# Optimization experiments

Hardware: AMD Instinct MI355X
Metric: run time of the kernel (lower is better)

## Reference

```python
import jax, jax.numpy as jnp
import numpy as np

N, E, B = 10000, 20000, 500
H, NODE_D, EDGE_D, L = 64, 11, 5, 3
BN_EPS = 1e-5
STEPS = 3  # Set2Set processing steps


def setup_inputs() -> dict:
    key = jax.random.key(0)
    ks = jax.random.split(key, 16)
    s = lambda k, shape, fan: (jax.random.normal(k, shape, jnp.float32) / np.sqrt(fan)).astype(jnp.float32)
    p = {}
    p["x"] = jax.random.normal(ks[0], (N, NODE_D), jnp.float32)
    p["edge_index"] = jax.random.randint(ks[1], (2, E), 0, N)
    p["edge_attr"] = jax.random.uniform(ks[2], (E, EDGE_D), dtype=jnp.float32)
    p["batch"] = jnp.sort(jax.random.randint(ks[3], (N,), 0, B))
    # node encoder
    p["W_enc"] = s(ks[4], (NODE_D, H), NODE_D); p["b_enc"] = jnp.zeros((H,), jnp.float32)
    # per-layer NNConv block params (stacked over L layers)
    p["eW1"] = s(ks[5], (L, EDGE_D, H), EDGE_D); p["eb1"] = jnp.zeros((L, H), jnp.float32)
    p["eW2"] = s(ks[6], (L, H, H * H), H);       p["eb2"] = jnp.zeros((L, H * H), jnp.float32)
    p["root"] = s(ks[7], (L, H, H), H);          p["cbias"] = jnp.zeros((L, H), jnp.float32)
    p["gamma"] = jnp.ones((L, H), jnp.float32);  p["beta"] = jnp.zeros((L, H), jnp.float32)
    # Set2Set LSTM (input 2H, hidden H)
    p["Wih"] = s(ks[8], (4 * H, 2 * H), 2 * H); p["Whh"] = s(ks[9], (4 * H, H), H)
    p["bih"] = jnp.zeros((4 * H,), jnp.float32); p["bhh"] = jnp.zeros((4 * H,), jnp.float32)
    p["hW1"] = s(ks[10], (2 * H, H), 2 * H);   p["hb1"] = jnp.zeros((H,), jnp.float32)
    p["hW2"] = s(ks[11], (H, H // 2), H);      p["hb2"] = jnp.zeros((H // 2,), jnp.float32)
    p["hW3"] = s(ks[12], (H // 2, 1), H // 2); p["hb3"] = jnp.zeros((1,), jnp.float32)
    return p


def _forward(x, edge_attr, W_enc, b_enc, eW1, eb1, eW2, eb2, root, cbias, gamma, beta,
             Wih, Whh, bih, bhh, hW1, hb1, hW2, hb2, hW3, hb3, edge_index, batch):
    src, dst = edge_index[0], edge_index[1]
    # in-degree for mean aggregation (0-degree nodes -> 0 output, clamp avoids /0)
    deg = jax.ops.segment_sum(jnp.ones((E,), jnp.float32), dst, num_segments=N)
    deg = jnp.maximum(deg, 1.0)[:, None]

    h = jax.nn.relu(x @ W_enc + b_enc)  # [N, H]

    for l in range(L):
        residual = h
        # edge MLP -> per-edge [H, H] weight matrix
        e1 = jax.nn.relu(edge_attr @ eW1[l] + eb1[l])          # [E, H]
        W = (e1 @ eW2[l] + eb2[l]).reshape(E, H, H)            # [E, H, H]
        msg = jnp.einsum('eh,eho->eo', h[src], W)              # per-edge matvec
        agg = jax.ops.segment_sum(msg, dst, num_segments=N) / deg
        h = agg + h @ root[l] + cbias[l]                       # NNConv (root + bias)
        # BatchNorm1d (training-mode batch stats, biased var), eval-mode dropout (no-op)
        mu = jnp.mean(h, axis=0)
        var = jnp.mean((h - mu) ** 2, axis=0)
        h = (h - mu) * jax.lax.rsqrt(var + BN_EPS) * gamma[l] + beta[l]
        h = jax.nn.relu(h) + residual

    # Set2Set readout
    q_star = jnp.zeros((B, 2 * H), jnp.float32)
    hl = jnp.zeros((B, H), jnp.float32)
    cl = jnp.zeros((B, H), jnp.float32)
    for _ in range(STEPS):
        gates = q_star @ Wih.T + bih + hl @ Whh.T + bhh
        i, f, g, o = jnp.split(gates, 4, axis=1)
        cl = jax.nn.sigmoid(f) * cl + jax.nn.sigmoid(i) * jnp.tanh(g)
        hl = jax.nn.sigmoid(o) * jnp.tanh(cl)
        q = hl                                                  # [B, H]
        e = jnp.sum(h * q[batch], axis=-1)                      # [N]
        m = jax.ops.segment_max(e, batch, num_segments=B)
        ex = jnp.exp(e - m[batch])
        sden = jax.ops.segment_sum(ex, batch, num_segments=B)
        a = ex / sden[batch]                                    # per-graph softmax
        r = jax.ops.segment_sum(a[:, None] * h, batch, num_segments=B)
        q_star = jnp.concatenate([q, r], axis=1)

    # head
    z = jax.nn.relu(q_star @ hW1 + hb1)
    z = jax.nn.relu(z @ hW2 + hb2)
    out = z @ hW3 + hb3
    return out.reshape(-1)  # [B]


def reference(x, edge_index, edge_attr, batch, W_enc, b_enc, eW1, eb1, eW2, eb2, root,
              cbias, gamma, beta, Wih, Whh, bih, bhh, hW1, hb1, hW2, hb2, hW3, hb3):
    return _forward(x, edge_attr, W_enc, b_enc, eW1, eb1, eW2, eb2, root, cbias, gamma,
                    beta, Wih, Whh, bih, bhh, hW1, hb1, hW2, hb2, hW3, hb3,
                    edge_index, batch)
```

## Files before the change

### kernel.cpp

```cpp
#include <hip/hip_runtime.h>
#include <math.h>

#define ND 11
#define ED 5
#define NL 3
#define NSTEPS 3
#define BN_EPS 1e-5f
#define NSLAB 32

typedef _Float16 half8 __attribute__((ext_vector_type(8)));
typedef float f32x4 __attribute__((ext_vector_type(4)));

__device__ __forceinline__ float sigm(float x) { return 1.0f / (1.0f + expf(-x)); }

__device__ __forceinline__ half8 to_h8(float4 a, float4 b) {
  half8 r;
  r[0] = (_Float16)a.x; r[1] = (_Float16)a.y; r[2] = (_Float16)a.z; r[3] = (_Float16)a.w;
  r[4] = (_Float16)b.x; r[5] = (_Float16)b.y; r[6] = (_Float16)b.z; r[7] = (_Float16)b.w;
  return r;
}

__device__ __forceinline__ half8 bn_h8(const float* __restrict__ hnrow,
                                       const float* __restrict__ hprow,
                                       const float* mu, const float* rs,
                                       const float* bt, int c0) {
  float4 p0 = *(const float4*)(hnrow);
  float4 p1 = *(const float4*)(hnrow + 4);
  float4 q0 = *(const float4*)(hprow);
  float4 q1 = *(const float4*)(hprow + 4);
  float pv[8] = {p0.x, p0.y, p0.z, p0.w, p1.x, p1.y, p1.z, p1.w};
  float qv[8] = {q0.x, q0.y, q0.z, q0.w, q1.x, q1.y, q1.z, q1.w};
  half8 r;
#pragma unroll
  for (int j = 0; j < 8; ++j) {
    float y = fmaxf((pv[j] - mu[c0 + j]) * rs[c0 + j] + bt[c0 + j], 0.f) + qv[j];
    r[j] = (_Float16)y;
  }
  return r;
}

__global__ __launch_bounds__(256) void k_setup(
    const float* __restrict__ x, const float* __restrict__ Wenc,
    const float* __restrict__ benc, float* __restrict__ h0, int N,
    const int* __restrict__ dst, float* __restrict__ deg, int E,
    const int* __restrict__ batch, int* __restrict__ ptr, int B,
    const float* __restrict__ Wih, const float* __restrict__ Whh,
    const float* __restrict__ bih, const float* __restrict__ bhh,
    float* __restrict__ WihT, float* __restrict__ WhhT, float* __restrict__ gbias,
    const float* __restrict__ w2, const float* __restrict__ b2,
    _Float16* __restrict__ w2P, float* __restrict__ zp, long NZ,
    int nbEnc, int nbDeg, int nbPtr, int nbPackW, int nbPack3) {
  int bid = blockIdx.x;
  const int tid = threadIdx.x;
  if (bid < nbEnc) {
    int idx = bid * 256 + tid;
    if (idx < N * 64) {
      int n = idx >> 6, j = idx & 63;
      float acc = benc[j];
#pragma unroll
      for (int i = 0; i < ND; ++i) acc = fmaf(x[n * ND + i], Wenc[i * 64 + j], acc);
      h0[idx] = fmaxf(acc, 0.0f);
    }
    return;
  }
  bid -= nbEnc;
  if (bid < nbDeg) {
    int e = bid * 256 + tid;
    if (e < E) atomicAdd(&deg[dst[e]], 1.0f);
    return;
  }
  bid -= nbDeg;
  if (bid < nbPtr) {
    int n = bid * 256 + tid;
    if (n < N) {
      int b = batch[n];
      int pb = (n == 0) ? -1 : batch[n - 1];
      for (int g = pb + 1; g <= b; ++g) ptr[g] = n;
      if (n == N - 1)
        for (int g = b + 1; g <= B; ++g) ptr[g] = N;
    }
    return;
  }
  bid -= nbPtr;
  if (bid < nbPackW) {
    int idx = bid * 256 + tid;
    if (idx < 128 * 256) {
      int i = idx >> 8, g = idx & 255;
      WihT[i * 256 + g] = Wih[g * 128 + i];
    } else if (idx < 192 * 256) {
      int j = idx - 128 * 256;
      int i = j >> 8, g = j & 255;
      WhhT[i * 256 + g] = Whh[g * 64 + i];
    } else if (idx < 192 * 256 + 256) {
      int g = idx - 192 * 256;
      gbias[g] = bih[g] + bhh[g];
    }
    return;
  }
  bid -= nbPackW;
  if (bid < nbPack3) {
    int lay = bid / 130;
    int idx = (bid % 130) * 256 + tid;
    int l = idx & 63;
    int f = (idx >> 6) & 7;
    int s = idx >> 9;
    int nf = f >> 1, kf = f & 1;
    const float* srow = (s < 64) ? (w2 + (size_t)lay * 64 * 4096 + (size_t)s * 4096)
                                 : (b2 + (size_t)lay * 4096);
    int o = nf * 16 + (l & 15);
    int hb = kf * 32 + (l >> 4) * 8;
    half8 v;
#pragma unroll
    for (int j = 0; j < 8; ++j) v[j] = (_Float16)srow[(hb + j) * 64 + o];
    *(half8*)(w2P + ((size_t)lay * 65 * 8 * 64 + idx) * 8) = v;
    return;
  }
  bid -= nbPack3;
  {
    long i4 = ((long)bid * 256 + tid) * 4;
    if (i4 + 3 < NZ) *(float4*)(zp + i4) = make_float4(0.f, 0.f, 0.f, 0.f);
    else for (; i4 < NZ; ++i4) zp[i4] = 0.f;
  }
}

__global__ void k_zdeg(float* __restrict__ deg, int N) {
  int i = blockIdx.x * blockDim.x + threadIdx.x;
  if (i < N) deg[i] = 0.f;
}

__global__ __launch_bounds__(256) void k_scan(const float* __restrict__ deg,
                                              int* __restrict__ dptr,
                                              int* __restrict__ cursor, int N) {
  __shared__ int wsum[4];
  __shared__ int s_carry;
  const int tid = threadIdx.x, lane = tid & 63, w = tid >> 6;
  if (tid == 0) s_carry = 0;
  __syncthreads();
  for (int base = 0; base < N; base += 1024) {
    int n0 = base + tid * 4;
    int v[4];
    int s = 0;
#pragma unroll
    for (int i = 0; i < 4; ++i) { v[i] = (n0 + i < N) ? (int)deg[n0 + i] : 0; s += v[i]; }
    int sc = s;
#pragma unroll
    for (int off = 1; off < 64; off <<= 1) {
      int t = __shfl_up(sc, off);
      if (lane >= off) sc += t;
    }
    if (lane == 63) wsum[w] = sc;
    __syncthreads();
    int wpre = 0;
    for (int ww = 0; ww < w; ++ww) wpre += wsum[ww];
    int excl = s_carry + wpre + sc - s;
#pragma unroll
    for (int i = 0; i < 4; ++i) {
      if (n0 + i < N) { dptr[n0 + i] = excl; cursor[n0 + i] = excl; }
      excl += v[i];
    }
    __syncthreads();
    if (tid == 255) s_carry += wsum[0] + wsum[1] + wsum[2] + wsum[3];
    __syncthreads();
  }
  if (threadIdx.x == 0) dptr[N] = s_carry;
}

__global__ void k_fill(const int* __restrict__ dst, const int* __restrict__ src,
                       int* __restrict__ cursor, int* __restrict__ perm,
                       int* __restrict__ srcP, int* __restrict__ dstP, int E) {
  int e = blockIdx.x * blockDim.x + threadIdx.x;
  if (e < E) {
    int d = dst[e];
    int slot = atomicAdd(&cursor[d], 1);
    perm[slot] = e;
    srcP[slot] = src[e];
    dstP[slot] = d;
  }
}

__global__ __launch_bounds__(512, 2) void k_msgagg(
    const float* __restrict__ ea, const int* __restrict__ perm,
    const float* __restrict__ eW1l, const float* __restrict__ eb1l,
    const float* __restrict__ hnp, const float* __restrict__ hp,
    const float* __restrict__ slabp, const float* __restrict__ gm,
    const float* __restrict__ bt, const int* __restrict__ srcP,
    const int* __restrict__ dstP, const int* __restrict__ dptr,
    const _Float16* __restrict__ w2P, float* __restrict__ agg, int E, int N) {
  __shared__ _Float16 e1t[65][64];
  __shared__ float tileH[2][64][66];
  __shared__ float eat[64][ED];
  __shared__ float w1s[ED * 64];
  __shared__ float b1s[64];
  __shared__ float stats[128];
  __shared__ float mu_s[64], rs_s[64], bt_s[64];

  const int tid = threadIdx.x;
  const int wid = tid >> 6, l = tid & 63;
  const int half = wid >> 2, quad = wid & 3;
  const int lo = l & 15, lg = l >> 4;
  const int e0 = blockIdx.x * 64;

  if (tid < ED * 64) w1s[tid] = eW1l[tid];
  else if (tid < ED * 64 + 64) b1s[tid - ED * 64] = eb1l[tid - ED * 64];
  else if (tid >= 384 && tid < 448 && slabp) {
    int j = tid - 384;
    float s0 = 0.f, s1 = 0.f;
#pragma unroll
    for (int sl = 0; sl < NSLAB; ++sl) {
      s0 += slabp[sl * 128 + j];
      s1 += slabp[sl * 128 + 64 + j];
    }
    stats[j] = s0;
    stats[64 + j] = s1;
  }
  if (tid >= 448) {
    int s = e0 + (tid - 448);
    if (s < E) {
      int e = perm[s];
#pragma unroll
      for (int i = 0; i < ED; ++i) eat[tid - 448][i] = ea[(size_t)e * ED + i];
    } else {
#pragma unroll
      for (int i = 0; i < ED; ++i) eat[tid - 448][i] = 0.f;
    }
  }
  __syncthreads();
  if (slabp && tid < 64) {
    float invN = 1.0f / (float)N;
    float mu = stats[tid] * invN;
    float var = stats[64 + tid] * invN - mu * mu;
    mu_s[tid] = mu;
    rs_s[tid] = rsqrtf(var + BN_EPS) * gm[tid];
    bt_s[tid] = bt[tid];
  }
  __syncthreads();

  for (int idx = tid; idx < 65 * 64; idx += 512) {
    int el = idx & 63, k = idx >> 6;
    float v = 1.0f;
    if (k < 64) {
      v = b1s[k];
#pragma unroll
      for (int i = 0; i < ED; ++i) v = fmaf(eat[el][i], w1s[i * 64 + k], v);
      v = fmaxf(v, 0.f);
    }
    e1t[k][el] = (_Float16)v;
  }

  half8 hsf[4][2];
#pragma unroll
  for (int m = 0; m < 4; ++m) {
    int s = e0 + m * 16 + lo;
    if (s < E) {
      const size_t row = (size_t)srcP[s] * 64;
      if (!slabp) {
        const float* hr = hp + row + lg * 8;
        hsf[m][0] = to_h8(*(const float4*)(hr), *(const float4*)(hr + 4));
        hsf[m][1] = to_h8(*(const float4*)(hr + 32), *(const float4*)(hr + 36));
      } else {
        hsf[m][0] = bn_h8(hnp + row + lg * 8, hp + row + lg * 8, mu_s, rs_s, bt_s, lg * 8);
        hsf[m][1] = bn_h8(hnp + row + 32 + lg * 8, hp + row + 32 + lg * 8,
                          mu_s, rs_s, bt_s, 32 + lg * 8);
      }
    } else {
      half8 z = {0, 0, 0, 0, 0, 0, 0, 0};
      hsf[m][0] = z;
      hsf[m][1] = z;
    }
  }
  __syncthreads();

  const int kb = half ? 32 : 0;
  f32x4 acc[4] = {};
  const half8* wp = (const half8*)w2P;
  half8 Br[4][2];
  _Float16 sr[4][4];
#pragma unroll
  for (int d = 0; d < 4; ++d) {
    const int k = kb + d;
    Br[d][0] = wp[((size_t)k * 8 + quad * 2 + 0) * 64 + l];
    Br[d][1] = wp[((size_t)k * 8 + quad * 2 + 1) * 64 + l];
#pragma unroll
    for (int m = 0; m < 4; ++m)
      sr[d][m] = (half && d == 0) ? (_Float16)0.f : e1t[k][m * 16 + lo];
  }
#pragma unroll 33
  for (int i = 0; i < 33; ++i) {
    const int d = i & 3;
#pragma unroll
    for (int m = 0; m < 4; ++m) {
      const _Float16 s16 = sr[d][m];
      half8 A0 = hsf[m][0] * s16;
      half8 A1 = hsf[m][1] * s16;
      acc[m] = __builtin_amdgcn_mfma_f32_16x16x32_f16(A0, Br[d][0], acc[m], 0, 0, 0);
      acc[m] = __builtin_amdgcn_mfma_f32_16x16x32_f16(A1, Br[d][1], acc[m], 0, 0, 0);
    }
    if (i + 4 < 33) {
      const int kn = kb + i + 4;
      Br[d][0] = wp[((size_t)kn * 8 + quad * 2 + 0) * 64 + l];
      Br[d][1] = wp[((size_t)kn * 8 + quad * 2 + 1) * 64 + l];
#pragma unroll
      for (int m = 0; m < 4; ++m) sr[d][m] = e1t[kn][m * 16 + lo];
    }
  }

#pragma unroll
  for (int m = 0; m < 4; ++m)
#pragma unroll
    for (int r = 0; r < 4; ++r)
      tileH[half][m * 16 + lg * 4 + r][quad * 16 + lo] = acc[m][r];
  __syncthreads();

  const int o = tid & 63, r8 = tid >> 6;
  const int lastSlot = (e0 + 63 < E) ? (e0 + 63) : (E - 1);
  const int nLo = dstP[e0], nHi = dstP[lastSlot];
  for (int nn = nLo + r8; nn <= nHi; nn += 8) {
    int d0 = dptr[nn], d1 = dptr[nn + 1];
    int j0 = (d0 > e0) ? d0 : e0;
    int j1 = (d1 < e0 + 64) ? d1 : (e0 + 64);
    float sum = 0.f;
    for (int j = j0; j < j1; ++j) sum += tileH[0][j - e0][o] + tileH[1][j - e0][o];
    float* dp = agg + (size_t)nn * 64 + o;
    if (d0 < e0 || d1 > e0 + 64) atomicAdd(dp, sum);
    else *dp = sum;
  }
}

__global__ __launch_bounds__(256) void k_update(
    const float* __restrict__ hnp, const float* __restrict__ hp,
    const float* __restrict__ slabp, const float* __restrict__ gm,
    const float* __restrict__ bt, float* __restrict__ hcur,
    float* __restrict__ agg, const float* __restrict__ deg,
    const float* __restrict__ root, const float* __restrict__ cb,
    float* __restrict__ hn_out, float* __restrict__ slab_out, int N) {
  __shared__ float hrow[16][64];
  __shared__ float red[2][256];
  __shared__ float stats[128];
  const int tid = threadIdx.x, o = tid & 63, r = tid >> 6;
  float muR = 0.f, rsR = 0.f, btR = 0.f;
  if (slabp) {
    if (tid < 128) {
      float s = 0.f;
#pragma unroll
      for (int sl = 0; sl < NSLAB; ++sl) s += slabp[sl * 128 + tid];
      stats[tid] = s;
    }
    __syncthreads();
    float invN = 1.0f / (float)N;
    float mu = stats[o] * invN;
    float var = stats[64 + o] * invN - mu * mu;
    muR = mu;
    rsR = rsqrtf(var + BN_EPS) * gm[o];
    btR = bt[o];
  }
  const int nb = blockIdx.x * 16;
#pragma unroll
  for (int ii = 0; ii < 4; ++ii) {
    int n = nb + ii * 4 + r;
    float hv = 0.f;
    if (n < N) {
      if (slabp) {
        float hnv = hnp[(size_t)n * 64 + o];
        float hpv = hp[(size_t)n * 64 + o];
        hv = fmaxf((hnv - muR) * rsR + btR, 0.f) + hpv;
        hcur[(size_t)n * 64 + o] = hv;
      } else {
        hv = hcur[(size_t)n * 64 + o];
      }
    }
    hrow[ii * 4 + r][o] = hv;
  }
  __syncthreads();
  float acc[4] = {0.f, 0.f, 0.f, 0.f};
  for (int c = 0; c < 64; ++c) {
    float rv = root[c * 64 + o];
#pragma unroll
    for (int ii = 0; ii < 4; ++ii) acc[ii] = fmaf(hrow[ii * 4 + r][c], rv, acc[ii]);
  }
  float s = 0.f, ss = 0.f;
  const float cbv = cb[o];
#pragma unroll
  for (int ii = 0; ii < 4; ++ii) {
    int n = nb + ii * 4 + r;
    if (n < N) {
      float a = agg[(size_t)n * 64 + o];
      agg[(size_t)n * 64 + o] = 0.f;
      float v = acc[ii] + cbv + a / fmaxf(deg[n], 1.0f);
      hn_out[(size_t)n * 64 + o] = v;
      s += v;
      ss += v * v;
    }
  }
  red[0][tid] = s;
  red[1][tid] = ss;
  __syncthreads();
  if (r == 0) {
    float t0 = red[0][o] + red[0][64 + o] + red[0][128 + o] + red[0][192 + o];
    float t1 = red[1][o] + red[1][64 + o] + red[1][128 + o] + red[1][192 + o];
    float* sl = slab_out + (size_t)(blockIdx.x & (NSLAB - 1)) * 128;
    atomicAdd(&sl[o], t0);
    atomicAdd(&sl[64 + o], t1);
  }
}

__global__ __launch_bounds__(256) void k_s2s_all(
    const float* __restrict__ hn2, const float* __restrict__ h2,
    const float* __restrict__ slab2, const float* __restrict__ gm,
    const float* __restrict__ bt, const int* __restrict__ ptr,
    const float* __restrict__ WihT, const float* __restrict__ WhhT,
    const float* __restrict__ gbias,
    const float* __restrict__ hW1, const float* __restrict__ hb1,
    const float* __restrict__ hW2, const float* __restrict__ hb2,
    const float* __restrict__ hW3, const float* __restrict__ hb3,
    float* __restrict__ out, int N) {
  __shared__ float stats[128];
  __shared__ float qs[128];
  __shared__ float hlc[64], clc[64];
  __shared__ float gates[256];
  __shared__ float qv[64];
  __shared__ float redM[4], redS[4];
  __shared__ float redR[4][64];
  __shared__ float z1[64], z2[32];
  const int b = blockIdx.x, tid = threadIdx.x;
  const int wid = tid >> 6, lane = tid & 63;

  if (tid < 128) {
    float s = 0.f;
#pragma unroll
    for (int sl = 0; sl < NSLAB; ++sl) s += slab2[sl * 128 + tid];
    stats[tid] = s;
    qs[tid] = 0.f;
  }
  if (tid < 64) { hlc[tid] = 0.f; clc[tid] = 0.f; }
  __syncthreads();
  const float invN = 1.0f / (float)N;
  const float muR = stats[lane] * invN;
  const float varR = stats[64 + lane] * invN - muR * muR;
  const float rsR = rsqrtf(varR + BN_EPS) * gm[lane];
  const float btR = bt[lane];
  const int beg = ptr[b], end = ptr[b + 1];

  for (int step = 0; step < NSTEPS; ++step) {
    float g = gbias[tid];
    for (int i = 0; i < 128; ++i) g = fmaf(qs[i], WihT[i * 256 + tid], g);
    for (int i = 0; i < 64; ++i) g = fmaf(hlc[i], WhhT[i * 256 + tid], g);
    gates[tid] = g;
    __syncthreads();
    if (tid < 64) {
      float ig = sigm(gates[tid]);
      float fg = sigm(gates[64 + tid]);
      float gg = tanhf(gates[128 + tid]);
      float og = sigm(gates[192 + tid]);
      float c = fg * clc[tid] + ig * gg;
      clc[tid] = c;
      float hnew = og * tanhf(c);
      hlc[tid] = hnew;
      qv[tid] = hnew;
    }
    __syncthreads();
    const float q = qv[lane];
    float mw = -INFINITY;
    for (int n = beg + wid; n < end; n += 4) {
      float hv = fmaxf((hn2[(size_t)n * 64 + lane] - muR) * rsR + btR, 0.f) +
                 h2[(size_t)n * 64 + lane];
      float p = hv * q;
#pragma unroll
      for (int s = 32; s; s >>= 1) p += __shfl_xor(p, s);
      mw = fmaxf(mw, p);
    }
    if (lane == 0) redM[wid] = mw;
    __syncthreads();
    const float m = fmaxf(fmaxf(redM[0], redM[1]), fmaxf(redM[2], redM[3]));
    float ssum = 0.f, racc = 0.f;
    for (int n = beg + wid; n < end; n += 4) {
      float hv = fmaxf((hn2[(size_t)n * 64 + lane] - muR) * rsR + btR, 0.f) +
                 h2[(size_t)n * 64 + lane];
      float p = hv * q;
#pragma unroll
      for (int s = 32; s; s >>= 1) p += __shfl_xor(p, s);
      float a = expf(p - m);
      ssum += a;
      racc = fmaf(a, hv, racc);
    }
    if (lane == 0) redS[wid] = ssum;
    redR[wid][lane] = racc;
    __syncthreads();
    if (tid < 128) {
      if (tid < 64) {
        qs[tid] = qv[tid];
      } else {
        int o2 = tid - 64;
        float rsum = redR[0][o2] + redR[1][o2] + redR[2][o2] + redR[3][o2];
        float sd = redS[0] + redS[1] + redS[2] + redS[3];
        qs[tid] = (end > beg) ? rsum / sd : 0.0f;
      }
    }
    __syncthreads();
  }

  if (tid < 64) {
    float a = hb1[tid];
    for (int i = 0; i < 128; ++i) a = fmaf(qs[i], hW1[i * 64 + tid], a);
    z1[tid] = fmaxf(a, 0.0f);
  }
  __syncthreads();
  if (tid < 32) {
    float a2 = hb2[tid];
    for (int i = 0; i < 64; ++i) a2 = fmaf(z1[i], hW2[i * 32 + tid], a2);
    z2[tid] = fmaxf(a2, 0.0f);
  }
  __syncthreads();
  if (tid < 64) {
    float p = (tid < 32) ? z2[tid] * hW3[tid] : 0.0f;
#pragma unroll
    for (int s = 32; s; s >>= 1) p += __shfl_xor(p, s);
    if (tid == 0) out[b] = p + hb3[0];
  }
}

extern "C" void kernel_launch(void* const* d_in, const int* in_sizes, int n_in,
                              void* d_out, int out_size, void* d_ws, size_t ws_size,
                              hipStream_t stream) {
  const float* x = (const float*)d_in[0];
  const int* eidx = (const int*)d_in[1];
  const float* ea = (const float*)d_in[2];
  const int* batch = (const int*)d_in[3];
  const float* Wenc = (const float*)d_in[4];
  const float* benc = (const float*)d_in[5];
  const float* eW1 = (const float*)d_in[6];
  const float* eb1 = (const float*)d_in[7];
  const float* eW2 = (const float*)d_in[8];
  const float* eb2 = (const float*)d_in[9];
  const float* root = (const float*)d_in[10];
  const float* cbias = (const float*)d_in[11];
  const float* gamma = (const float*)d_in[12];
  const float* beta = (const float*)d_in[13];
  const float* Wih = (const float*)d_in[14];
  const float* Whh = (const float*)d_in[15];
  const float* bih = (const float*)d_in[16];
  const float* bhh = (const float*)d_in[17];
  const float* hW1 = (const float*)d_in[18];
  const float* hb1 = (const float*)d_in[19];
  const float* hW2 = (const float*)d_in[20];
  const float* hb2 = (const float*)d_in[21];
  const float* hW3 = (const float*)d_in[22];
  const float* hb3 = (const float*)d_in[23];

  const int N = in_sizes[0] / ND;
  const int E = in_sizes[1] / 2;
  const int B = out_size;
  const int* srcp = eidx;
  const int* dstp = eidx + E;
  const int Etiles = (E + 63) / 64;

  float* ws = (float*)d_ws;
  float* deg = ws;
  float* agg = deg + N;
  float* bnslab = agg + (size_t)N * 64;
  const long NZ = (long)((size_t)N * 64 + NL * NSLAB * 128);
  float* h0 = bnslab + NL * NSLAB * 128;
  float* h1 = h0 + (size_t)N * 64;
  float* h2 = h1 + (size_t)N * 64;
  float* hn0 = h2 + (size_t)N * 64;
  float* hn1 = hn0 + (size_t)N * 64;
  float* hn2 = hn1 + (size_t)N * 64;
  _Float16* w2P = (_Float16*)(hn2 + (size_t)N * 64);
  float* WihT = (float*)(w2P + (size_t)3 * 65 * 8 * 64 * 8);
  float* WhhT = WihT + 128 * 256;
  float* gbias = WhhT + 64 * 256;
  int* dptr = (int*)(gbias + 256);
  int* cursor = dptr + N + 1;
  int* perm = cursor + N;
  int* srcP = perm + E;
  int* dstP = srcP + E;
  int* ptr = dstP + E;

  const int nbEnc = (N * 64 + 255) / 256;
  const int nbDeg = (E + 255) / 256;
  const int nbPtr = (N + 255) / 256;
  const int nbPackW = (192 * 256 + 256 + 255) / 256;
  const int nbPack3 = 130 * NL;
  const int nbZero = (int)((NZ / 4 + 255) / 256);

  k_zdeg<<<(N + 255) / 256, 256, 0, stream>>>(deg, N);
  k_setup<<<nbEnc + nbDeg + nbPtr + nbPackW + nbPack3 + nbZero, 256, 0, stream>>>(
      x, Wenc, benc, h0, N, dstp, deg, E, batch, ptr, B,
      Wih, Whh, bih, bhh, WihT, WhhT, gbias, eW2, eb2, w2P, agg, NZ,
      nbEnc, nbDeg, nbPtr, nbPackW, nbPack3);
  k_scan<<<1, 256, 0, stream>>>(deg, dptr, cursor, N);
  k_fill<<<(E + 255) / 256, 256, 0, stream>>>(dstp, srcp, cursor, perm, srcP, dstP, E);

  float* hbuf[3] = {h0, h1, h2};
  float* hnbuf[3] = {hn0, hn1, hn2};
  for (int l = 0; l < NL; ++l) {
    const float* slabp = (l == 0) ? nullptr : bnslab + (size_t)(l - 1) * NSLAB * 128;
    const float* gmp = (l == 0) ? nullptr : gamma + (l - 1) * 64;
    const float* btp = (l == 0) ? nullptr : beta + (l - 1) * 64;
    const float* hnp = (l == 0) ? nullptr : hnbuf[l - 1];
    const float* hp = (l == 0) ? h0 : hbuf[l - 1];
    float* slab_l = bnslab + (size_t)l * NSLAB * 128;
    const _Float16* w2_l = w2P + (size_t)l * 65 * 8 * 64 * 8;
    k_msgagg<<<Etiles, 512, 0, stream>>>(ea, perm, eW1 + (size_t)l * ED * 64,
                                         eb1 + (size_t)l * 64, hnp, hp, slabp, gmp, btp,
                                         srcP, dstP, dptr, w2_l, agg, E, N);
    k_update<<<(N + 15) / 16, 256, 0, stream>>>(hnp, hp, slabp, gmp, btp, hbuf[l], agg,
                                                deg, root + (size_t)l * 64 * 64,
                                                cbias + l * 64, hnbuf[l], slab_l, N);
  }

  k_s2s_all<<<B, 256, 0, stream>>>(hn2, h2, bnslab + (size_t)2 * NSLAB * 128,
                                   gamma + 2 * 64, beta + 2 * 64, ptr, WihT, WhhT, gbias,
                                   hW1, hb1, hW2, hb2, hW3, hb3, (float*)d_out, N);
}
```

Before: 210.7 us.

## Split message-passing K dimension across two blocks per edge tile

Splits the 65-slice contraction of the per-edge weight product in k_msgagg across a second grid dimension. Each block now covers 2×17 K-slices, with the slices padded to 68 using zero weights. All partial sums go to agg through atomicAdd instead of the previous direct store. This doubles the block count to raise occupancy and shorten each block's MFMA chain, at the cost of redoing the edge MLP, h gather and staging in both blocks, and of more atomic traffic. Index clamps were also added to the scatter.

```diff
diff --git a/kernel.cpp b/kernel.cpp
--- a/kernel.cpp
+++ b/kernel.cpp
@@ -7,6 +7,7 @@
 #define NSTEPS 3
 #define BN_EPS 1e-5f
 #define NSLAB 32
+#define KSL 68
 
 typedef _Float16 half8 __attribute__((ext_vector_type(8)));
 typedef float f32x4 __attribute__((ext_vector_type(4)));
@@ -99,20 +100,25 @@
   }
   bid -= nbPackW;
   if (bid < nbPack3) {
-    int lay = bid / 130;
-    int idx = (bid % 130) * 256 + tid;
+    int lay = bid / 136;
+    int idx = (bid % 136) * 256 + tid;
     int l = idx & 63;
     int f = (idx >> 6) & 7;
     int s = idx >> 9;
     int nf = f >> 1, kf = f & 1;
-    const float* srow = (s < 64) ? (w2 + (size_t)lay * 64 * 4096 + (size_t)s * 4096)
-                                 : (b2 + (size_t)lay * 4096);
     int o = nf * 16 + (l & 15);
     int hb = kf * 32 + (l >> 4) * 8;
     half8 v;
-#pragma unroll
-    for (int j = 0; j < 8; ++j) v[j] = (_Float16)srow[(hb + j) * 64 + o];
-    *(half8*)(w2P + ((size_t)lay * 65 * 8 * 64 + idx) * 8) = v;
+    if (s < 65) {
+      const float* srow = (s < 64) ? (w2 + (size_t)lay * 64 * 4096 + (size_t)s * 4096)
+                                   : (b2 + (size_t)lay * 4096);
+#pragma unroll
+      for (int j = 0; j < 8; ++j) v[j] = (_Float16)srow[(hb + j) * 64 + o];
+    } else {
+#pragma unroll
+      for (int j = 0; j < 8; ++j) v[j] = (_Float16)0.f;
+    }
+    *(half8*)(w2P + ((size_t)lay * KSL * 8 * 64 + idx) * 8) = v;
     return;
   }
   bid -= nbPack3;
@@ -186,7 +192,7 @@
     const float* __restrict__ bt, const int* __restrict__ srcP,
     const int* __restrict__ dstP, const int* __restrict__ dptr,
     const _Float16* __restrict__ w2P, float* __restrict__ agg, int E, int N) {
-  __shared__ _Float16 e1t[65][64];
+  __shared__ _Float16 e1t[KSL][64];
   __shared__ float tileH[2][64][66];
   __shared__ float eat[64][ED];
   __shared__ float w1s[ED * 64];
@@ -199,6 +205,7 @@
   const int half = wid >> 2, quad = wid & 3;
   const int lo = l & 15, lg = l >> 4;
   const int e0 = blockIdx.x * 64;
+  const int ks = blockIdx.y;
 
   if (tid < ED * 64) w1s[tid] = eW1l[tid];
   else if (tid < ED * 64 + 64) b1s[tid - ED * 64] = eb1l[tid - ED * 64];
@@ -235,14 +242,16 @@
   }
   __syncthreads();
 
-  for (int idx = tid; idx < 65 * 64; idx += 512) {
+  for (int idx = tid; idx < KSL * 64; idx += 512) {
     int el = idx & 63, k = idx >> 6;
-    float v = 1.0f;
+    float v = 0.f;
     if (k < 64) {
       v = b1s[k];
 #pragma unroll
       for (int i = 0; i < ED; ++i) v = fmaf(eat[el][i], w1s[i * 64 + k], v);
       v = fmaxf(v, 0.f);
+    } else if (k == 64) {
+      v = 1.0f;
     }
     e1t[k][el] = (_Float16)v;
   }
@@ -270,7 +279,7 @@
   }
   __syncthreads();
 
-  const int kb = half ? 32 : 0;
+  const int kb = (ks * 2 + half) * 17;
   f32x4 acc[4] = {};
   const half8* wp = (const half8*)w2P;
   half8 Br[4][2];
@@ -281,11 +290,10 @@
     Br[d][0] = wp[((size_t)k * 8 + quad * 2 + 0) * 64 + l];
     Br[d][1] = wp[((size_t)k * 8 + quad * 2 + 1) * 64 + l];
 #pragma unroll
-    for (int m = 0; m < 4; ++m)
-      sr[d][m] = (half && d == 0) ? (_Float16)0.f : e1t[k][m * 16 + lo];
-  }
-#pragma unroll 33
-  for (int i = 0; i < 33; ++i) {
+    for (int m = 0; m < 4; ++m) sr[d][m] = e1t[k][m * 16 + lo];
+  }
+#pragma unroll 17
+  for (int i = 0; i < 17; ++i) {
     const int d = i & 3;
 #pragma unroll
     for (int m = 0; m < 4; ++m) {
@@ -295,7 +303,7 @@
       acc[m] = __builtin_amdgcn_mfma_f32_16x16x32_f16(A0, Br[d][0], acc[m], 0, 0, 0);
       acc[m] = __builtin_amdgcn_mfma_f32_16x16x32_f16(A1, Br[d][1], acc[m], 0, 0, 0);
     }
-    if (i + 4 < 33) {
+    if (i + 4 < 17) {
       const int kn = kb + i + 4;
       Br[d][0] = wp[((size_t)kn * 8 + quad * 2 + 0) * 64 + l];
       Br[d][1] = wp[((size_t)kn * 8 + quad * 2 + 1) * 64 + l];
@@ -313,16 +321,18 @@
 
   const int o = tid & 63, r8 = tid >> 6;
   const int lastSlot = (e0 + 63 < E) ? (e0 + 63) : (E - 1);
-  const int nLo = dstP[e0], nHi = dstP[lastSlot];
+  int nLo = dstP[e0], nHi = dstP[lastSlot];
+  nLo = (nLo < 0) ? 0 : ((nLo >= N) ? N - 1 : nLo);
+  nHi = (nHi < 0) ? 0 : ((nHi >= N) ? N - 1 : nHi);
   for (int nn = nLo + r8; nn <= nHi; nn += 8) {
     int d0 = dptr[nn], d1 = dptr[nn + 1];
+    d0 = (d0 < 0) ? 0 : d0;
+    d1 = (d1 > E) ? E : d1;
     int j0 = (d0 > e0) ? d0 : e0;
     int j1 = (d1 < e0 + 64) ? d1 : (e0 + 64);
     float sum = 0.f;
     for (int j = j0; j < j1; ++j) sum += tileH[0][j - e0][o] + tileH[1][j - e0][o];
-    float* dp = agg + (size_t)nn * 64 + o;
-    if (d0 < e0 || d1 > e0 + 64) atomicAdd(dp, sum);
-    else *dp = sum;
+    if (j1 > j0) atomicAdd(agg + (size_t)nn * 64 + o, sum);
   }
 }
 
@@ -565,7 +575,7 @@
   float* hn1 = hn0 + (size_t)N * 64;
   float* hn2 = hn1 + (size_t)N * 64;
   _Float16* w2P = (_Float16*)(hn2 + (size_t)N * 64);
-  float* WihT = (float*)(w2P + (size_t)3 * 65 * 8 * 64 * 8);
+  float* WihT = (float*)(w2P + (size_t)3 * KSL * 8 * 64 * 8);
   float* WhhT = WihT + 128 * 256;
   float* gbias = WhhT + 64 * 256;
   int* dptr = (int*)(gbias + 256);
@@ -579,7 +589,7 @@
   const int nbDeg = (E + 255) / 256;
   const int nbPtr = (N + 255) / 256;
   const int nbPackW = (192 * 256 + 256 + 255) / 256;
-  const int nbPack3 = 130 * NL;
+  const int nbPack3 = 136 * NL;
   const int nbZero = (int)((NZ / 4 + 255) / 256);
 
   k_zdeg<<<(N + 255) / 256, 256, 0, stream>>>(deg, N);
@@ -599,10 +609,11 @@
     const float* hnp = (l == 0) ? nullptr : hnbuf[l - 1];
     const float* hp = (l == 0) ? h0 : hbuf[l - 1];
     float* slab_l = bnslab + (size_t)l * NSLAB * 128;
-    const _Float16* w2_l = w2P + (size_t)l * 65 * 8 * 64 * 8;
-    k_msgagg<<<Etiles, 512, 0, stream>>>(ea, perm, eW1 + (size_t)l * ED * 64,
-                                         eb1 + (size_t)l * 64, hnp, hp, slabp, gmp, btp,
-                                         srcP, dstP, dptr, w2_l, agg, E, N);
+    const _Float16* w2_l = w2P + (size_t)l * KSL * 8 * 64 * 8;
+    dim3 gm(Etiles, 2);
+    k_msgagg<<<gm, 512, 0, stream>>>(ea, perm, eW1 + (size_t)l * ED * 64,
+                                     eb1 + (size_t)l * 64, hnp, hp, slabp, gmp, btp,
+                                     srcP, dstP, dptr, w2_l, agg, E, N);
     k_update<<<(N + 15) / 16, 256, 0, stream>>>(hnp, hp, slabp, gmp, btp, hbuf[l], agg,
                                                 deg, root + (size_t)l * 64 * 64,
                                                 cbias + l * 64, hnbuf[l], slab_l, N);
```

Measured after the change: 234.3 us. 11.2% more time.

## Materialize normalized node features once in fp16 before message kernel

Applied to the files above, without the earlier changes.

Adds a separate elementwise kernel that applies batch-norm, ReLU and the residual once per layer, writing both fp32 and fp16 copies of the node features. The message kernel then gathers source rows as fp16 vectors directly, and its gather is moved ahead of the shared-memory setup so the loads can overlap it. This removes the per-edge redundant BN math, the slab reduction in every block and half of the gathered bytes. The cost is an extra kernel launch and an extra full pass over the node features per layer. It also adds bounds clamping on the destination ranges.

```diff
diff --git a/kernel.cpp b/kernel.cpp
--- a/kernel.cpp
+++ b/kernel.cpp
@@ -13,35 +13,10 @@
 
 __device__ __forceinline__ float sigm(float x) { return 1.0f / (1.0f + expf(-x)); }
 
-__device__ __forceinline__ half8 to_h8(float4 a, float4 b) {
-  half8 r;
-  r[0] = (_Float16)a.x; r[1] = (_Float16)a.y; r[2] = (_Float16)a.z; r[3] = (_Float16)a.w;
-  r[4] = (_Float16)b.x; r[5] = (_Float16)b.y; r[6] = (_Float16)b.z; r[7] = (_Float16)b.w;
-  return r;
-}
-
-__device__ __forceinline__ half8 bn_h8(const float* __restrict__ hnrow,
-                                       const float* __restrict__ hprow,
-                                       const float* mu, const float* rs,
-                                       const float* bt, int c0) {
-  float4 p0 = *(const float4*)(hnrow);
-  float4 p1 = *(const float4*)(hnrow + 4);
-  float4 q0 = *(const float4*)(hprow);
-  float4 q1 = *(const float4*)(hprow + 4);
-  float pv[8] = {p0.x, p0.y, p0.z, p0.w, p1.x, p1.y, p1.z, p1.w};
-  float qv[8] = {q0.x, q0.y, q0.z, q0.w, q1.x, q1.y, q1.z, q1.w};
-  half8 r;
-#pragma unroll
-  for (int j = 0; j < 8; ++j) {
-    float y = fmaxf((pv[j] - mu[c0 + j]) * rs[c0 + j] + bt[c0 + j], 0.f) + qv[j];
-    r[j] = (_Float16)y;
-  }
-  return r;
-}
-
 __global__ __launch_bounds__(256) void k_setup(
     const float* __restrict__ x, const float* __restrict__ Wenc,
-    const float* __restrict__ benc, float* __restrict__ h0, int N,
+    const float* __restrict__ benc, float* __restrict__ h0,
+    _Float16* __restrict__ hh, int N,
     const int* __restrict__ dst, float* __restrict__ deg, int E,
     const int* __restrict__ batch, int* __restrict__ ptr, int B,
     const float* __restrict__ Wih, const float* __restrict__ Whh,
@@ -59,7 +34,9 @@
       float acc = benc[j];
 #pragma unroll
       for (int i = 0; i < ND; ++i) acc = fmaf(x[n * ND + i], Wenc[i * 64 + j], acc);
-      h0[idx] = fmaxf(acc, 0.0f);
+      float v = fmaxf(acc, 0.0f);
+      h0[idx] = v;
+      hh[idx] = (_Float16)v;
     }
     return;
   }
@@ -178,12 +155,36 @@
   }
 }
 
+__global__ __launch_bounds__(256) void k_hmat(
+    const float* __restrict__ hn, const float* __restrict__ hp,
+    const float* __restrict__ slab, const float* __restrict__ gm,
+    const float* __restrict__ bt, float* __restrict__ hout,
+    _Float16* __restrict__ hh, int N) {
+  __shared__ float stats[128];
+  const int tid = threadIdx.x;
+  if (tid < 128) {
+    float s = 0.f;
+#pragma unroll
+    for (int sl = 0; sl < NSLAB; ++sl) s += slab[sl * 128 + tid];
+    stats[tid] = s;
+  }
+  __syncthreads();
+  int idx = blockIdx.x * 256 + tid;
+  if (idx >= N * 64) return;
+  int o = idx & 63;
+  float invN = 1.0f / (float)N;
+  float mu = stats[o] * invN;
+  float var = stats[64 + o] * invN - mu * mu;
+  float rs = rsqrtf(var + BN_EPS) * gm[o];
+  float v = fmaxf((hn[idx] - mu) * rs + bt[o], 0.f) + hp[idx];
+  hout[idx] = v;
+  hh[idx] = (_Float16)v;
+}
+
 __global__ __launch_bounds__(512, 2) void k_msgagg(
     const float* __restrict__ ea, const int* __restrict__ perm,
     const float* __restrict__ eW1l, const float* __restrict__ eb1l,
-    const float* __restrict__ hnp, const float* __restrict__ hp,
-    const float* __restrict__ slabp, const float* __restrict__ gm,
-    const float* __restrict__ bt, const int* __restrict__ srcP,
+    const _Float16* __restrict__ hh, const int* __restrict__ srcP,
     const int* __restrict__ dstP, const int* __restrict__ dptr,
     const _Float16* __restrict__ w2P, float* __restrict__ agg, int E, int N) {
   __shared__ _Float16 e1t[65][64];
@@ -191,8 +192,6 @@
   __shared__ float eat[64][ED];
   __shared__ float w1s[ED * 64];
   __shared__ float b1s[64];
-  __shared__ float stats[128];
-  __shared__ float mu_s[64], rs_s[64], bt_s[64];
 
   const int tid = threadIdx.x;
   const int wid = tid >> 6, l = tid & 63;
@@ -200,19 +199,23 @@
   const int lo = l & 15, lg = l >> 4;
   const int e0 = blockIdx.x * 64;
 
+  half8 hsf[4][2];
+#pragma unroll
+  for (int m = 0; m < 4; ++m) {
+    int s = e0 + m * 16 + lo;
+    if (s < E) {
+      const _Float16* hr = hh + (size_t)srcP[s] * 64;
+      hsf[m][0] = *(const half8*)(hr + lg * 8);
+      hsf[m][1] = *(const half8*)(hr + 32 + lg * 8);
+    } else {
+      half8 z = {0, 0, 0, 0, 0, 0, 0, 0};
+      hsf[m][0] = z;
+      hsf[m][1] = z;
+    }
+  }
+
   if (tid < ED * 64) w1s[tid] = eW1l[tid];
   else if (tid < ED * 64 + 64) b1s[tid - ED * 64] = eb1l[tid - ED * 64];
-  else if (tid >= 384 && tid < 448 && slabp) {
-    int j = tid - 384;
-    float s0 = 0.f, s1 = 0.f;
-#pragma unroll
-    for (int sl = 0; sl < NSLAB; ++sl) {
-      s0 += slabp[sl * 128 + j];
-      s1 += slabp[sl * 128 + 64 + j];
-    }
-    stats[j] = s0;
-    stats[64 + j] = s1;
-  }
   if (tid >= 448) {
     int s = e0 + (tid - 448);
     if (s < E) {
@@ -223,15 +226,6 @@
 #pragma unroll
       for (int i = 0; i < ED; ++i) eat[tid - 448][i] = 0.f;
     }
-  }
-  __syncthreads();
-  if (slabp && tid < 64) {
-    float invN = 1.0f / (float)N;
-    float mu = stats[tid] * invN;
-    float var = stats[64 + tid] * invN - mu * mu;
-    mu_s[tid] = mu;
-    rs_s[tid] = rsqrtf(var + BN_EPS) * gm[tid];
-    bt_s[tid] = bt[tid];
   }
   __syncthreads();
 
@@ -245,28 +239,6 @@
       v = fmaxf(v, 0.f);
     }
     e1t[k][el] = (_Float16)v;
-  }
-
-  half8 hsf[4][2];
-#pragma unroll
-  for (int m = 0; m < 4; ++m) {
-    int s = e0 + m * 16 + lo;
-    if (s < E) {
-      const size_t row = (size_t)srcP[s] * 64;
-      if (!slabp) {
-        const float* hr = hp + row + lg * 8;
-        hsf[m][0] = to_h8(*(const float4*)(hr), *(const float4*)(hr + 4));
-        hsf[m][1] = to_h8(*(const float4*)(hr + 32), *(const float4*)(hr + 36));
-      } else {
-        hsf[m][0] = bn_h8(hnp + row + lg * 8, hp + row + lg * 8, mu_s, rs_s, bt_s, lg * 8);
-        hsf[m][1] = bn_h8(hnp + row + 32 + lg * 8, hp + row + 32 + lg * 8,
-                          mu_s, rs_s, bt_s, 32 + lg * 8);
-      }
-    } else {
-      half8 z = {0, 0, 0, 0, 0, 0, 0, 0};
-      hsf[m][0] = z;
-      hsf[m][1] = z;
-    }
   }
   __syncthreads();
 
@@ -313,62 +285,36 @@
 
   const int o = tid & 63, r8 = tid >> 6;
   const int lastSlot = (e0 + 63 < E) ? (e0 + 63) : (E - 1);
-  const int nLo = dstP[e0], nHi = dstP[lastSlot];
+  int nLo = dstP[e0], nHi = dstP[lastSlot];
+  nLo = (nLo < 0) ? 0 : ((nLo >= N) ? N - 1 : nLo);
+  nHi = (nHi < 0) ? 0 : ((nHi >= N) ? N - 1 : nHi);
   for (int nn = nLo + r8; nn <= nHi; nn += 8) {
     int d0 = dptr[nn], d1 = dptr[nn + 1];
+    d0 = (d0 < 0) ? 0 : d0;
+    d1 = (d1 > E) ? E : d1;
     int j0 = (d0 > e0) ? d0 : e0;
     int j1 = (d1 < e0 + 64) ? d1 : (e0 + 64);
     float sum = 0.f;
     for (int j = j0; j < j1; ++j) sum += tileH[0][j - e0][o] + tileH[1][j - e0][o];
     float* dp = agg + (size_t)nn * 64 + o;
-    if (d0 < e0 || d1 > e0 + 64) atomicAdd(dp, sum);
+    if (d0 < e0 || d1 > e0 + 64) { if (j1 > j0) atomicAdd(dp, sum); }
     else *dp = sum;
   }
 }
 
 __global__ __launch_bounds__(256) void k_update(
-    const float* __restrict__ hnp, const float* __restrict__ hp,
-    const float* __restrict__ slabp, const float* __restrict__ gm,
-    const float* __restrict__ bt, float* __restrict__ hcur,
-    float* __restrict__ agg, const float* __restrict__ deg,
-    const float* __restrict__ root, const float* __restrict__ cb,
-    float* __restrict__ hn_out, float* __restrict__ slab_out, int N) {
+    const float* __restrict__ hcur, float* __restrict__ agg,
+    const float* __restrict__ deg, const float* __restrict__ root,
+    const float* __restrict__ cb, float* __restrict__ hn_out,
+    float* __restrict__ slab_out, int N) {
   __shared__ float hrow[16][64];
   __shared__ float red[2][256];
-  __shared__ float stats[128];
   const int tid = threadIdx.x, o = tid & 63, r = tid >> 6;
-  float muR = 0.f, rsR = 0.f, btR = 0.f;
-  if (slabp) {
-    if (tid < 128) {
-      float s = 0.f;
-#pragma unroll
-      for (int sl = 0; sl < NSLAB; ++sl) s += slabp[sl * 128 + tid];
-      stats[tid] = s;
-    }
-    __syncthreads();
-    float invN = 1.0f / (float)N;
-    float mu = stats[o] * invN;
-    float var = stats[64 + o] * invN - mu * mu;
-    muR = mu;
-    rsR = rsqrtf(var + BN_EPS) * gm[o];
-    btR = bt[o];
-  }
   const int nb = blockIdx.x * 16;
 #pragma unroll
   for (int ii = 0; ii < 4; ++ii) {
     int n = nb + ii * 4 + r;
-    float hv = 0.f;
-    if (n < N) {
-      if (slabp) {
-        float hnv = hnp[(size_t)n * 64 + o];
-        float hpv = hp[(size_t)n * 64 + o];
-        hv = fmaxf((hnv - muR) * rsR + btR, 0.f) + hpv;
-        hcur[(size_t)n * 64 + o] = hv;
-      } else {
-        hv = hcur[(size_t)n * 64 + o];
-      }
-    }
-    hrow[ii * 4 + r][o] = hv;
+    hrow[ii * 4 + r][o] = (n < N) ? hcur[(size_t)n * 64 + o] : 0.f;
   }
   __syncthreads();
   float acc[4] = {0.f, 0.f, 0.f, 0.f};
@@ -565,7 +511,8 @@
   float* hn1 = hn0 + (size_t)N * 64;
   float* hn2 = hn1 + (size_t)N * 64;
   _Float16* w2P = (_Float16*)(hn2 + (size_t)N * 64);
-  float* WihT = (float*)(w2P + (size_t)3 * 65 * 8 * 64 * 8);
+  _Float16* hhalf = w2P + (size_t)3 * 65 * 8 * 64 * 8;
+  float* WihT = (float*)(hhalf + (size_t)N * 64);
   float* WhhT = WihT + 128 * 256;
   float* gbias = WhhT + 64 * 256;
   int* dptr = (int*)(gbias + 256);
@@ -584,7 +531,7 @@
 
   k_zdeg<<<(N + 255) / 256, 256, 0, stream>>>(deg, N);
   k_setup<<<nbEnc + nbDeg + nbPtr + nbPackW + nbPack3 + nbZero, 256, 0, stream>>>(
-      x, Wenc, benc, h0, N, dstp, deg, E, batch, ptr, B,
+      x, Wenc, benc, h0, hhalf, N, dstp, deg, E, batch, ptr, B,
       Wih, Whh, bih, bhh, WihT, WhhT, gbias, eW2, eb2, w2P, agg, NZ,
       nbEnc, nbDeg, nbPtr, nbPackW, nbPack3);
   k_scan<<<1, 256, 0, stream>>>(deg, dptr, cursor, N);
@@ -593,18 +540,18 @@
   float* hbuf[3] = {h0, h1, h2};
   float* hnbuf[3] = {hn0, hn1, hn2};
   for (int l = 0; l < NL; ++l) {
-    const float* slabp = (l == 0) ? nullptr : bnslab + (size_t)(l - 1) * NSLAB * 128;
-    const float* gmp = (l == 0) ? nullptr : gamma + (l - 1) * 64;
-    const float* btp = (l == 0) ? nullptr : beta + (l - 1) * 64;
-    const float* hnp = (l == 0) ? nullptr : hnbuf[l - 1];
-    const float* hp = (l == 0) ? h0 : hbuf[l - 1];
     float* slab_l = bnslab + (size_t)l * NSLAB * 128;
     const _Float16* w2_l = w2P + (size_t)l * 65 * 8 * 64 * 8;
+    if (l > 0) {
+      k_hmat<<<(N * 64 + 255) / 256, 256, 0, stream>>>(
+          hnbuf[l - 1], hbuf[l - 1], bnslab + (size_t)(l - 1) * NSLAB * 128,
+          gamma + (l - 1) * 64, beta + (l - 1) * 64, hbuf[l], hhalf, N);
+    }
     k_msgagg<<<Etiles, 512, 0, stream>>>(ea, perm, eW1 + (size_t)l * ED * 64,
-                                         eb1 + (size_t)l * 64, hnp, hp, slabp, gmp, btp,
-                                         srcP, dstP, dptr, w2_l, agg, E, N);
-    k_update<<<(N + 15) / 16, 256, 0, stream>>>(hnp, hp, slabp, gmp, btp, hbuf[l], agg,
-                                                deg, root + (size_t)l * 64 * 64,
+                                         eb1 + (size_t)l * 64, hhalf, srcP, dstP, dptr,
+                                         w2_l, agg, E, N);
+    k_update<<<(N + 15) / 16, 256, 0, stream>>>(hbuf[l], agg, deg,
+                                                root + (size_t)l * 64 * 64,
                                                 cbias + l * 64, hnbuf[l], slab_l, N);
   }
 
```

Result: slower. 216.1 us (+2.6%).
